# Performance work log

Hardware: AMD Instinct MI355X
Metric: run time of the kernel (lower is better)

The kernel has to match this reference:

```python
import jax, jax.numpy as jnp
import numpy as np


def _discretize(A, B, C, step):
    # Bilinear (Tustin) discretization, as in the source module.
    N = A.shape[0]
    I = jnp.eye(N, dtype=A.dtype)
    BL = jnp.linalg.inv(I - (step / 2.0) * A)
    Ab = BL @ (I + (step / 2.0) * A)
    Bb = (BL * step) @ B  # (N, 1)
    return Ab, Bb, C


def _k_conv(Ab, Bb, Cb, L):
    # K[l] = Cb @ Ab^l @ Bb, computed by a linear recurrence instead of
    # L explicit matrix powers (same math as the source's K_conv).
    def step(v, _):
        k = (Cb @ v)[0, 0]
        return Ab @ v, k

    _, K = jax.lax.scan(step, Bb, None, length=L)
    return K  # (L,)


def setup_inputs() -> dict:
    key = jax.random.key(0)
    k_u, k_a, k_b, k_c, k_s = jax.random.split(key, 5)
    N, L, BATCH = 64, 16384, 512
    u = jax.random.normal(k_u, (BATCH, L), dtype=jnp.float32)
    # lecun_normal inits: std = 1/sqrt(fan_in)
    A = jax.random.normal(k_a, (N, N), dtype=jnp.float32) / np.sqrt(N)
    B = jax.random.normal(k_b, (N, 1), dtype=jnp.float32)  # fan_in = 1
    C = jax.random.normal(k_c, (1, N), dtype=jnp.float32) / np.sqrt(N)
    D = jnp.ones((1,), dtype=jnp.float32)
    # log_step_initializer(dt_min=1e-3, dt_max=0.1)
    lo, hi = np.log(1e-3), np.log(0.1)
    log_step = (jax.random.uniform(k_s, (1,)) * (hi - lo) + lo).astype(jnp.float32)
    return {"u": u, "A": A, "B": B, "C": C, "D": D, "log_step": log_step}


def reference(u, A, B, C, D, log_step) -> jnp.ndarray:
    L = u.shape[-1]
    step = jnp.exp(log_step)  # (1,)
    Ab, Bb, Cb = _discretize(A, B, C, step)
    K = _k_conv(Ab, Bb, Cb, L)  # (L,)
    # FFT causal convolution: pad both signals to length 2L (as in source),
    # multiply in frequency domain, take first L samples.
    n = 2 * L
    ud = jnp.fft.rfft(u, n=n, axis=-1)          # (BATCH, L+1) complex
    Kd = jnp.fft.rfft(K, n=n)                   # (L+1,) complex, broadcast
    y = jnp.fft.irfft(ud * Kd, n=n, axis=-1)[..., :L]
    return y + D * u
```

## Files before the change

### kernel.cpp

```cpp
#include <hip/hip_runtime.h>
#include <cstddef>

typedef double f64x4 __attribute__((ext_vector_type(4)));
typedef float  f32x4 __attribute__((ext_vector_type(4)));
typedef short  bf16x8 __attribute__((ext_vector_type(8)));

static constexpr int RCN = 512 * 128;

static constexpr size_t WS_W  = 0;
static constexpr size_t WS_G  = 8192;
static constexpr size_t WS_MD = 32768;
static constexpr size_t WS_BV = 40960;
static constexpr size_t WS_X  = WS_BV + (size_t)RCN * 64;

__device__ __forceinline__ unsigned short f2bf(float f) {
  union { float f; unsigned u; } v; v.f = f;
  unsigned u = v.u + 0x7FFFu + ((v.u >> 16) & 1u);
  return (unsigned short)(u >> 16);
}

__device__ __forceinline__ double probeE(int i, int k) {
  return (double)(((i * 3 + k * 5) & 7) - 3);
}
__device__ __forceinline__ double probeF(int k, int j) {
  return (double)(((k * 7 + j * 2) & 7) - 4);
}

__device__ __forceinline__ bool probe_mfma_layout(int lr, int lq, int rowm[4], int* colm_out)
{
  f64x4 z; z[0] = 0.0; z[1] = 0.0; z[2] = 0.0; z[3] = 0.0;
  f64x4 p1 = __builtin_amdgcn_mfma_f64_16x16x4f64((double)lr, 1.0, z, 0, 0, 0);
  f64x4 p2 = __builtin_amdgcn_mfma_f64_16x16x4f64(1.0, (double)lr, z, 0, 0, 0);
  bool okl = true;
#pragma unroll
  for (int r = 0; r < 4; ++r) {
    int rr = (int)(p1[r] * 0.25 + 0.5);
    okl = okl && (p1[r] == 4.0 * (double)rr) && rr >= 0 && rr < 16;
    rowm[r] = rr & 15;
    okl = okl && (p2[r] == p2[0]);
  }
  int cc = (int)(p2[0] * 0.25 + 0.5);
  okl = okl && (p2[0] == 4.0 * (double)cc) && cc >= 0 && cc < 16;
  *colm_out = cc & 15;
  f64x4 d = __builtin_amdgcn_mfma_f64_16x16x4f64(probeE(lr, lq), probeF(lq, lr), z, 0, 0, 0);
#pragma unroll
  for (int r = 0; r < 4; ++r) {
    double ref = 0.0;
#pragma unroll
    for (int k = 0; k < 4; ++k) ref += probeE(rowm[r], k) * probeF(k, cc & 15);
    okl = okl && (d[r] == ref);
  }
  return __all(okl) != 0;
}

template<bool ADD>
__device__ __forceinline__ void mm64_mfma(const double* A, const double* B, double* D,
                                          int wi, int wj, int lr, int lq,
                                          const int rowm[4], int colm)
{
  f64x4 acc;
  if (ADD) {
#pragma unroll
    for (int r = 0; r < 4; ++r)
      acc[r] = D[(wi * 16 + rowm[r]) * 65 + wj * 16 + colm];
  } else {
    acc[0] = 0.0; acc[1] = 0.0; acc[2] = 0.0; acc[3] = 0.0;
  }
#pragma unroll
  for (int kb = 0; kb < 16; ++kb) {
    double a = A[(wi * 16 + lr) * 65 + kb * 4 + lq];
    double b = B[(kb * 4 + lq) * 65 + wj * 16 + lr];
    acc = __builtin_amdgcn_mfma_f64_16x16x4f64(a, b, acc, 0, 0, 0);
  }
  __syncthreads();
#pragma unroll
  for (int r = 0; r < 4; ++r)
    D[(wi * 16 + rowm[r]) * 65 + wj * 16 + colm] = acc[r];
  __syncthreads();
}

__device__ __forceinline__ void wh_tile(const float* Wf, const float* Hf,
                                        const double* Pd, float* Wo, float* Ho,
                                        int n, bool isW, int wi, int wj,
                                        int lr, int lq, const int rowm[4], int colm)
{
  f64x4 acc;
  acc[0] = 0.0; acc[1] = 0.0; acc[2] = 0.0; acc[3] = 0.0;
#pragma unroll
  for (int kb = 0; kb < 16; ++kb) {
    double a, b;
    if (isW) {
      a = (double)Wf[(wi * 16 + lr) * 65 + kb * 4 + lq];
      b = Pd[(wj * 16 + lr) * 65 + kb * 4 + lq];
    } else {
      a = (double)Hf[(wi * 16 + lr) * 65 + kb * 4 + lq];
      b = Pd[(kb * 4 + lq) * 65 + wj * 16 + lr];
    }
    acc = __builtin_amdgcn_mfma_f64_16x16x4f64(a, b, acc, 0, 0, 0);
  }
#pragma unroll
  for (int r = 0; r < 4; ++r) {
    int drow = wi * 16 + rowm[r];
    if (drow < n) {
      if (isW) Wo[(n + drow) * 65 + wj * 16 + colm] = (float)acc[r];
      else     Ho[(n + drow) * 65 + wj * 16 + colm] = (float)acc[r];
    }
  }
}

template<bool ADD>
__device__ __forceinline__ void mm64x2(const double* A, const double* B, double* D,
                                       int tr2, int tc2)
{
  double a00 = 0, a01 = 0, a10 = 0, a11 = 0;
#pragma unroll 8
  for (int c = 0; c < 64; ++c) {
    double av0 = A[(tr2 + 0) * 65 + c];
    double av1 = A[(tr2 + 1) * 65 + c];
    double bv0 = B[c * 65 + tc2 + 0];
    double bv1 = B[c * 65 + tc2 + 1];
    a00 = fma(av0, bv0, a00); a01 = fma(av0, bv1, a01);
    a10 = fma(av1, bv0, a10); a11 = fma(av1, bv1, a11);
  }
  double o00, o01, o10, o11;
  if (ADD) {
    o00 = D[(tr2 + 0) * 65 + tc2 + 0]; o01 = D[(tr2 + 0) * 65 + tc2 + 1];
    o10 = D[(tr2 + 1) * 65 + tc2 + 0]; o11 = D[(tr2 + 1) * 65 + tc2 + 1];
  }
  __syncthreads();
  D[(tr2 + 0) * 65 + tc2 + 0] = ADD ? (o00 + a00) : a00;
  D[(tr2 + 0) * 65 + tc2 + 1] = ADD ? (o01 + a01) : a01;
  D[(tr2 + 1) * 65 + tc2 + 0] = ADD ? (o10 + a10) : a10;
  D[(tr2 + 1) * 65 + tc2 + 1] = ADD ? (o11 + a11) : a11;
  __syncthreads();
}

__global__ __launch_bounds__(1024) void k_precomp(
    const float* __restrict__ Ain, const float* __restrict__ Bin,
    const float* __restrict__ Cin, const float* __restrict__ Din,
    const float* __restrict__ LS, float* ws)
{
  __shared__ double Xd[64 * 65];
  __shared__ double Pd[64 * 65];
  __shared__ float  Wf[128 * 65];
  __shared__ float  Hf[128 * 65];
  __shared__ float  Kf[128];

  const int t    = threadIdx.x;
  const int wave = t >> 6;
  const int lane = t & 63;
  const int lr   = lane & 15;
  const int lq   = lane >> 4;
  const int wv_i = wave >> 2;
  const int wv_j = wave & 3;
  const int tr2  = (t >> 5) << 1;
  const int tc2  = (t & 31) << 1;

  int rowm[4]; int colm;
  const bool use_mfma = probe_mfma_layout(lr, lq, rowm, &colm);

  unsigned short* Wtg = (unsigned short*)(ws + WS_W);
  unsigned short* Gtg = (unsigned short*)(ws + WS_G);
  double* Mgd = (double*)(ws + WS_MD);

  const double step = exp((double)LS[0]);
  const double h = 0.5 * step;

  for (int idx = t; idx < 4096; idx += 1024) {
    int i = idx >> 6, j = idx & 63;
    double a = h * (double)Ain[idx];
    Xd[i * 65 + j] = a;
    Pd[i * 65 + j] = a + ((i == j) ? 1.0 : 0.0);
  }
  __syncthreads();

  if (use_mfma) {
    for (int k = 0; k < 3; ++k) {
      mm64_mfma<false>(Xd, Xd, Xd, wv_i, wv_j, lr, lq, rowm, colm);
      mm64_mfma<true >(Pd, Xd, Pd, wv_i, wv_j, lr, lq, rowm, colm);
    }
  } else {
    for (int k = 0; k < 3; ++k) {
      mm64x2<false>(Xd, Xd, Xd, tr2, tc2);
      mm64x2<true >(Pd, Xd, Pd, tr2, tc2);
    }
  }

  if (t < 64) {
    double bb = 0.0;
    for (int c = 0; c < 64; ++c) bb = fma(Pd[t * 65 + c], (double)Bin[c], bb);
    Wf[t] = (float)(bb * step);
  }
  __syncthreads();

  for (int idx = t; idx < 4096; idx += 1024) {
    int i = idx >> 6, j = idx & 63;
    Pd[i * 65 + j] = 2.0 * Pd[i * 65 + j] - ((i == j) ? 1.0 : 0.0);
  }
  __syncthreads();

  if (t < 64) {
    double hh = 0.0;
    for (int c = 0; c < 64; ++c) hh = fma((double)Cin[c], Pd[c * 65 + t], hh);
    Hf[t] = (float)hh;
  }
  __syncthreads();

  if (use_mfma) {
    for (int k = 0; k < 7; ++k) {
      const int n     = 1 << k;
      const int tpm   = (n + 15) >> 4;
      const int tiles = tpm << 2;
      if (tiles <= 8) {
        if (wave < 2 * tiles) {
          const bool isW = wave < tiles;
          const int  w   = isW ? wave : wave - tiles;
          wh_tile(Wf, Hf, Pd, Wf, Hf, n, isW, w >> 2, w & 3, lr, lq, rowm, colm);
        }
      } else {
        wh_tile(Wf, Hf, Pd, Wf, Hf, n, true,  wv_i, wv_j, lr, lq, rowm, colm);
        wh_tile(Wf, Hf, Pd, Wf, Hf, n, false, wv_i, wv_j, lr, lq, rowm, colm);
      }
      mm64_mfma<false>(Pd, Pd, Pd, wv_i, wv_j, lr, lq, rowm, colm);
    }
  } else {
    for (int k = 0; k < 7; ++k) {
      const int n = 1 << k;
      if (n <= 16) {
        if (t < (n << 6)) {
          int r = t >> 6, ii = t & 63;
          double aw = 0.0, ah = 0.0;
#pragma unroll 4
          for (int c = 0; c < 64; ++c) {
            aw = fma(Pd[ii * 65 + c], (double)Wf[r * 65 + c], aw);
            ah = fma((double)Hf[r * 65 + c], Pd[c * 65 + ii], ah);
          }
          Wf[(n + r) * 65 + ii] = (float)aw;
          Hf[(n + r) * 65 + ii] = (float)ah;
        }
      } else if (n == 32) {
        const int r  = t >> 5;
        const int i2 = (t & 31) << 1;
        double w0 = 0, w1 = 0, h0 = 0, h1 = 0;
#pragma unroll 4
        for (int c = 0; c < 64; ++c) {
          double wr = (double)Wf[r * 65 + c];
          w0 = fma(wr, Pd[(i2 + 0) * 65 + c], w0);
          w1 = fma(wr, Pd[(i2 + 1) * 65 + c], w1);
          double hr = (double)Hf[r * 65 + c];
          h0 = fma(hr, Pd[c * 65 + i2 + 0], h0);
          h1 = fma(hr, Pd[c * 65 + i2 + 1], h1);
        }
        Wf[(32 + r) * 65 + i2 + 0] = (float)w0;
        Wf[(32 + r) * 65 + i2 + 1] = (float)w1;
        Hf[(32 + r) * 65 + i2 + 0] = (float)h0;
        Hf[(32 + r) * 65 + i2 + 1] = (float)h1;
      } else {
        const int r2 = tr2, i2 = tc2;
        double w00 = 0, w01 = 0, w10 = 0, w11 = 0;
        double h00 = 0, h01 = 0, h10 = 0, h11 = 0;
#pragma unroll 4
        for (int c = 0; c < 64; ++c) {
          double wa = (double)Wf[(r2 + 0) * 65 + c];
          double wb = (double)Wf[(r2 + 1) * 65 + c];
          double p0 = Pd[(i2 + 0) * 65 + c];
          double p1 = Pd[(i2 + 1) * 65 + c];
          w00 = fma(wa, p0, w00); w01 = fma(wa, p1, w01);
          w10 = fma(wb, p0, w10); w11 = fma(wb, p1, w11);
          double ha = (double)Hf[(r2 + 0) * 65 + c];
          double hb = (double)Hf[(r2 + 1) * 65 + c];
          double q0 = Pd[c * 65 + i2 + 0];
          double q1 = Pd[c * 65 + i2 + 1];
          h00 = fma(ha, q0, h00); h01 = fma(ha, q1, h01);
          h10 = fma(hb, q0, h10); h11 = fma(hb, q1, h11);
        }
        Wf[(64 + r2 + 0) * 65 + i2 + 0] = (float)w00;
        Wf[(64 + r2 + 0) * 65 + i2 + 1] = (float)w01;
        Wf[(64 + r2 + 1) * 65 + i2 + 0] = (float)w10;
        Wf[(64 + r2 + 1) * 65 + i2 + 1] = (float)w11;
        Hf[(64 + r2 + 0) * 65 + i2 + 0] = (float)h00;
        Hf[(64 + r2 + 0) * 65 + i2 + 1] = (float)h01;
        Hf[(64 + r2 + 1) * 65 + i2 + 0] = (float)h10;
        Hf[(64 + r2 + 1) * 65 + i2 + 1] = (float)h11;
      }
      mm64x2<false>(Pd, Pd, Pd, tr2, tc2);
    }
  }

  for (int idx = t; idx < 4096; idx += 1024)
    Mgd[idx] = Pd[(idx >> 6) * 65 + (idx & 63)];

  if (t < 128) {
    double s = 0.0;
    for (int c = 0; c < 64; ++c) s = fma((double)Cin[c], (double)Wf[t * 65 + c], s);
    Kf[t] = (float)s;
  }
  __syncthreads();

  for (int idx = t; idx < 8192; idx += 1024) {
    int i = idx >> 7, kk = idx & 127;
    Wtg[idx] = f2bf(Wf[(127 - kk) * 65 + i]);
  }

  const float Dval = Din[0];
  for (int idx = t; idx < 16384; idx += 1024) {
    int r = idx >> 7, kg = idx & 127;
    float v = (r >= kg) ? Kf[r - kg] : 0.f;
    if (kg == r) v += Dval;
    Gtg[r * 192 + kg] = f2bf(v);
  }
  for (int idx = t; idx < 8192; idx += 1024) {
    int r = idx >> 6, i = idx & 63;
    Gtg[r * 192 + 128 + i] = f2bf(Hf[r * 65 + i]);
  }
}

__global__ __launch_bounds__(256) void k_chunkvec(
    const float* __restrict__ u, const unsigned short* __restrict__ Wt,
    float* __restrict__ bout)
{
  __shared__ unsigned short Bs[64 * 136];
  __shared__ unsigned short As[128 * 40];
  const int t = threadIdx.x;
  const int rc0 = blockIdx.x << 7;
  const int w  = t >> 6;
  const int lane = t & 63;
  const int lr = lane & 15, lq = lane >> 4;

  {
    const unsigned* src = (const unsigned*)Wt;
    unsigned* dst = (unsigned*)Bs;
    for (int idx = t; idx < 4096; idx += 256) {
      int r = idx >> 6, c = idx & 63;
      dst[r * 68 + c] = src[idx];
    }
  }
  for (int it = t; it < 1024; it += 256) {
    int rcl = it >> 3, k4 = (it & 7) << 2;
    float4 v = *(const float4*)&u[((size_t)(rc0 + rcl) << 7) + k4];
    ushort4 s;
    s.x = f2bf(v.x); s.y = f2bf(v.y); s.z = f2bf(v.z); s.w = f2bf(v.w);
    *(ushort4*)&As[rcl * 40 + k4] = s;
  }
  __syncthreads();

  f32x4 acc[2][4];
#pragma unroll
  for (int i = 0; i < 2; ++i)
#pragma unroll
    for (int j = 0; j < 4; ++j) { acc[i][j][0] = 0.f; acc[i][j][1] = 0.f; acc[i][j][2] = 0.f; acc[i][j][3] = 0.f; }

  for (int sl = 0; sl < 4; ++sl) {
    bf16x8 av[2], bv[4];
#pragma unroll
    for (int ti = 0; ti < 2; ++ti)
      av[ti] = *(const bf16x8*)&As[(w * 32 + ti * 16 + lr) * 40 + lq * 8];
#pragma unroll
    for (int tj = 0; tj < 4; ++tj)
      bv[tj] = *(const bf16x8*)&Bs[(tj * 16 + lr) * 136 + sl * 32 + lq * 8];
#pragma unroll
    for (int ti = 0; ti < 2; ++ti)
#pragma unroll
      for (int tj = 0; tj < 4; ++tj)
        acc[ti][tj] = __builtin_amdgcn_mfma_f32_16x16x32_bf16(av[ti], bv[tj], acc[ti][tj], 0, 0, 0);
    if (sl < 3) {
      __syncthreads();
      for (int it = t; it < 1024; it += 256) {
        int rcl = it >> 3, k4 = (it & 7) << 2;
        float4 v = *(const float4*)&u[((size_t)(rc0 + rcl) << 7) + ((sl + 1) << 5) + k4];
        ushort4 s;
        s.x = f2bf(v.x); s.y = f2bf(v.y); s.z = f2bf(v.z); s.w = f2bf(v.w);
        *(ushort4*)&As[rcl * 40 + k4] = s;
      }
      __syncthreads();
    }
  }

#pragma unroll
  for (int ti = 0; ti < 2; ++ti)
#pragma unroll
    for (int tj = 0; tj < 4; ++tj)
#pragma unroll
      for (int r = 0; r < 4; ++r) {
        int row = rc0 + w * 32 + ti * 16 + lq * 4 + r;
        bout[((size_t)row << 6) + tj * 16 + lr] = acc[ti][tj][r];
      }
}

__global__ __launch_bounds__(64) void k_scan(
    const double* __restrict__ Mg, const float* __restrict__ bv,
    float* __restrict__ Xg)
{
  __shared__ float xs[64];
  const int lane = threadIdx.x;
  float Mr[64];
#pragma unroll
  for (int c = 0; c < 64; ++c)
    Mr[c] = (float)Mg[((size_t)lane << 6) + c];
  const float* br = bv + ((size_t)blockIdx.x << 13);
  float* Xr = Xg + ((size_t)blockIdx.x << 13);
  xs[lane] = 0.f;
  float bcur = br[lane];
  __syncthreads();
  for (int j = 0; j < 128; ++j) {
    float bnext = (j < 127) ? br[((j + 1) << 6) + lane] : 0.f;
    float y0 = 0.f, y1 = 0.f, y2 = 0.f, y3 = 0.f;
#pragma unroll
    for (int c4 = 0; c4 < 16; ++c4) {
      float4 xv = *(const float4*)&xs[c4 << 2];
      y0 = fmaf(Mr[c4 * 4 + 0], xv.x, y0);
      y1 = fmaf(Mr[c4 * 4 + 1], xv.y, y1);
      y2 = fmaf(Mr[c4 * 4 + 2], xv.z, y2);
      y3 = fmaf(Mr[c4 * 4 + 3], xv.w, y3);
    }
    float xold = xs[lane];
    Xr[(j << 6) + lane] = xold;
    float xnew = bcur + ((y0 + y1) + (y2 + y3));
    __syncthreads();
    xs[lane] = xnew;
    __syncthreads();
    bcur = bnext;
  }
}

__global__ __launch_bounds__(256) void k_main(
    const float* __restrict__ u, const float* __restrict__ Xg,
    const unsigned short* __restrict__ Gt, float* __restrict__ out)
{
  __shared__ unsigned short Gs[128 * 200];
  __shared__ unsigned short As[128 * 40];
  const int t = threadIdx.x;
  const int rc0 = blockIdx.x << 7;
  const int w  = t >> 6;
  const int lane = t & 63;
  const int lr = lane & 15, lq = lane >> 4;

  {
    const unsigned* src = (const unsigned*)Gt;
    unsigned* dst = (unsigned*)Gs;
    for (int idx = t; idx < 12288; idx += 256) {
      int r = idx / 96, c = idx - r * 96;
      dst[r * 100 + c] = src[idx];
    }
  }
  for (int it = t; it < 1024; it += 256) {
    int rcl = it >> 3, k4 = (it & 7) << 2;
    float4 v = *(const float4*)&u[((size_t)(rc0 + rcl) << 7) + k4];
    ushort4 s;
    s.x = f2bf(v.x); s.y = f2bf(v.y); s.z = f2bf(v.z); s.w = f2bf(v.w);
    *(ushort4*)&As[rcl * 40 + k4] = s;
  }
  __syncthreads();

  f32x4 acc[2][8];
#pragma unroll
  for (int i = 0; i < 2; ++i)
#pragma unroll
    for (int j = 0; j < 8; ++j) { acc[i][j][0] = 0.f; acc[i][j][1] = 0.f; acc[i][j][2] = 0.f; acc[i][j][3] = 0.f; }

  for (int sl = 0; sl < 6; ++sl) {
    bf16x8 av[2], bv[8];
#pragma unroll
    for (int ti = 0; ti < 2; ++ti)
      av[ti] = *(const bf16x8*)&As[(w * 32 + ti * 16 + lr) * 40 + lq * 8];
#pragma unroll
    for (int tj = 0; tj < 8; ++tj)
      bv[tj] = *(const bf16x8*)&Gs[(tj * 16 + lr) * 200 + sl * 32 + lq * 8];
#pragma unroll
    for (int ti = 0; ti < 2; ++ti)
#pragma unroll
      for (int tj = 0; tj < 8; ++tj)
        acc[ti][tj] = __builtin_amdgcn_mfma_f32_16x16x32_bf16(av[ti], bv[tj], acc[ti][tj], 0, 0, 0);
    if (sl < 5) {
      __syncthreads();
      for (int it = t; it < 1024; it += 256) {
        int rcl = it >> 3, k4 = (it & 7) << 2;
        int kg = ((sl + 1) << 5) + k4;
        float4 v;
        if (kg < 128)
          v = *(const float4*)&u[((size_t)(rc0 + rcl) << 7) + kg];
        else
          v = *(const float4*)&Xg[((size_t)(rc0 + rcl) << 6) + (kg - 128)];
        ushort4 s;
        s.x = f2bf(v.x); s.y = f2bf(v.y); s.z = f2bf(v.z); s.w = f2bf(v.w);
        *(ushort4*)&As[rcl * 40 + k4] = s;
      }
      __syncthreads();
    }
  }

#pragma unroll
  for (int ti = 0; ti < 2; ++ti)
#pragma unroll
    for (int tj = 0; tj < 8; ++tj)
#pragma unroll
      for (int r = 0; r < 4; ++r) {
        int row = rc0 + w * 32 + ti * 16 + lq * 4 + r;
        out[((size_t)row << 7) + tj * 16 + lr] = acc[ti][tj][r];
      }
}

extern "C" void kernel_launch(void* const* d_in, const int* in_sizes, int n_in,
                              void* d_out, int out_size, void* d_ws, size_t ws_size,
                              hipStream_t stream) {
  (void)in_sizes; (void)n_in; (void)out_size; (void)ws_size;
  const float* u  = (const float*)d_in[0];
  const float* A  = (const float*)d_in[1];
  const float* Bv = (const float*)d_in[2];
  const float* Cv = (const float*)d_in[3];
  const float* Dv = (const float*)d_in[4];
  const float* ls = (const float*)d_in[5];
  float* out = (float*)d_out;
  float* ws  = (float*)d_ws;

  k_precomp<<<1, 1024, 0, stream>>>(A, Bv, Cv, Dv, ls, ws);
  k_chunkvec<<<512, 256, 0, stream>>>(u, (const unsigned short*)(ws + WS_W), ws + WS_BV);
  k_scan<<<512, 64, 0, stream>>>((const double*)(ws + WS_MD), ws + WS_BV, ws + WS_X);
  k_main<<<512, 256, 0, stream>>>(u, ws + WS_X, (const unsigned short*)(ws + WS_G), out);
}
```

Baseline: 220.5 us.

## Halve serial chunk scan depth via squared transition matrix and pairwise combining

The chunk-state scan now pairs adjacent chunks. Each pair is combined in parallel with M, then a single wave runs a 64-step serial recurrence using M^2, which is precomputed in k_precomp. Odd states are reconstructed in parallel afterwards. Cross-lane access uses readlane instead of shared-memory syncs, and the block uses 256 threads with chunk inputs staged in LDS. M is now stored as float rather than double, which lowers precision slightly, and the squared matrix adds some rounding error.

```diff
diff --git a/kernel.cpp b/kernel.cpp
--- a/kernel.cpp
+++ b/kernel.cpp
@@ -161,7 +161,7 @@
 
   unsigned short* Wtg = (unsigned short*)(ws + WS_W);
   unsigned short* Gtg = (unsigned short*)(ws + WS_G);
-  double* Mgd = (double*)(ws + WS_MD);
+  float* Mf = ws + WS_MD;
 
   const double step = exp((double)LS[0]);
   const double h = 0.5 * step;
@@ -288,7 +288,12 @@
   }
 
   for (int idx = t; idx < 4096; idx += 1024)
-    Mgd[idx] = Pd[(idx >> 6) * 65 + (idx & 63)];
+    Mf[idx] = (float)Pd[(idx >> 6) * 65 + (idx & 63)];
+
+  if (use_mfma) mm64_mfma<false>(Pd, Pd, Pd, wv_i, wv_j, lr, lq, rowm, colm);
+  else          mm64x2<false>(Pd, Pd, Pd, tr2, tc2);
+  for (int idx = t; idx < 4096; idx += 1024)
+    Mf[4096 + idx] = (float)Pd[(idx >> 6) * 65 + (idx & 63)];
 
   if (t < 128) {
     double s = 0.0;
@@ -387,39 +392,78 @@
       }
 }
 
-__global__ __launch_bounds__(64) void k_scan(
-    const double* __restrict__ Mg, const float* __restrict__ bv,
-    float* __restrict__ Xg)
-{
-  __shared__ float xs[64];
-  const int lane = threadIdx.x;
-  float Mr[64];
-#pragma unroll
-  for (int c = 0; c < 64; ++c)
-    Mr[c] = (float)Mg[((size_t)lane << 6) + c];
+__global__ __launch_bounds__(256) void k_scan(
+    const float* __restrict__ Mf,
+    const float* __restrict__ bv, float* __restrict__ Xg)
+{
+  __shared__ float bs[128 * 64];
+  __shared__ float ds[64 * 64];
+  __shared__ float xs[64 * 64];
+  const int t = threadIdx.x, w = t >> 6, lane = t & 63;
   const float* br = bv + ((size_t)blockIdx.x << 13);
   float* Xr = Xg + ((size_t)blockIdx.x << 13);
-  xs[lane] = 0.f;
-  float bcur = br[lane];
-  __syncthreads();
-  for (int j = 0; j < 128; ++j) {
-    float bnext = (j < 127) ? br[((j + 1) << 6) + lane] : 0.f;
+
+  for (int it = t; it < 2048; it += 256)
+    ((float4*)bs)[it] = ((const float4*)br)[it];
+
+  float Mr[64], M2r[64];
+#pragma unroll
+  for (int c4 = 0; c4 < 16; ++c4) {
+    *(float4*)&Mr[c4 * 4]  = *(const float4*)&Mf[(lane << 6) + c4 * 4];
+    *(float4*)&M2r[c4 * 4] = *(const float4*)&Mf[4096 + (lane << 6) + c4 * 4];
+  }
+  __syncthreads();
+
+  for (int k = 0; k < 16; ++k) {
+    const int tp = (w << 4) + k;
     float y0 = 0.f, y1 = 0.f, y2 = 0.f, y3 = 0.f;
 #pragma unroll
     for (int c4 = 0; c4 < 16; ++c4) {
-      float4 xv = *(const float4*)&xs[c4 << 2];
-      y0 = fmaf(Mr[c4 * 4 + 0], xv.x, y0);
-      y1 = fmaf(Mr[c4 * 4 + 1], xv.y, y1);
-      y2 = fmaf(Mr[c4 * 4 + 2], xv.z, y2);
-      y3 = fmaf(Mr[c4 * 4 + 3], xv.w, y3);
-    }
-    float xold = xs[lane];
-    Xr[(j << 6) + lane] = xold;
-    float xnew = bcur + ((y0 + y1) + (y2 + y3));
-    __syncthreads();
-    xs[lane] = xnew;
-    __syncthreads();
-    bcur = bnext;
+      float4 bb = *(const float4*)&bs[((tp << 1) << 6) + (c4 << 2)];
+      y0 = fmaf(Mr[c4 * 4 + 0], bb.x, y0);
+      y1 = fmaf(Mr[c4 * 4 + 1], bb.y, y1);
+      y2 = fmaf(Mr[c4 * 4 + 2], bb.z, y2);
+      y3 = fmaf(Mr[c4 * 4 + 3], bb.w, y3);
+    }
+    ds[(tp << 6) + lane] = ((y0 + y1) + (y2 + y3)) + bs[(((tp << 1) + 1) << 6) + lane];
+  }
+  __syncthreads();
+
+  if (w == 0) {
+    float x = 0.f;
+    float ecur = ds[lane];
+    for (int u = 0; u < 64; ++u) {
+      xs[(u << 6) + lane] = x;
+      float en = (u < 63) ? ds[((u + 1) << 6) + lane] : 0.f;
+      const unsigned xb = __float_as_uint(x);
+      float y0 = 0.f, y1 = 0.f, y2 = 0.f, y3 = 0.f;
+#pragma unroll
+      for (int c = 0; c < 64; c += 4) {
+        y0 = fmaf(M2r[c + 0], __uint_as_float(__builtin_amdgcn_readlane(xb, c + 0)), y0);
+        y1 = fmaf(M2r[c + 1], __uint_as_float(__builtin_amdgcn_readlane(xb, c + 1)), y1);
+        y2 = fmaf(M2r[c + 2], __uint_as_float(__builtin_amdgcn_readlane(xb, c + 2)), y2);
+        y3 = fmaf(M2r[c + 3], __uint_as_float(__builtin_amdgcn_readlane(xb, c + 3)), y3);
+      }
+      x = ((y0 + y1) + (y2 + y3)) + ecur;
+      ecur = en;
+    }
+  }
+  __syncthreads();
+
+  for (int k = 0; k < 16; ++k) {
+    const int tp = (w << 4) + k;
+    Xr[((tp << 1) << 6) + lane] = xs[(tp << 6) + lane];
+    float y0 = 0.f, y1 = 0.f, y2 = 0.f, y3 = 0.f;
+#pragma unroll
+    for (int c4 = 0; c4 < 16; ++c4) {
+      float4 xx = *(const float4*)&xs[(tp << 6) + (c4 << 2)];
+      y0 = fmaf(Mr[c4 * 4 + 0], xx.x, y0);
+      y1 = fmaf(Mr[c4 * 4 + 1], xx.y, y1);
+      y2 = fmaf(Mr[c4 * 4 + 2], xx.z, y2);
+      y3 = fmaf(Mr[c4 * 4 + 3], xx.w, y3);
+    }
+    Xr[(((tp << 1) + 1) << 6) + lane] =
+        ((y0 + y1) + (y2 + y3)) + bs[((tp << 1) << 6) + lane];
   }
 }
 
@@ -515,6 +559,6 @@
 
   k_precomp<<<1, 1024, 0, stream>>>(A, Bv, Cv, Dv, ls, ws);
   k_chunkvec<<<512, 256, 0, stream>>>(u, (const unsigned short*)(ws + WS_W), ws + WS_BV);
-  k_scan<<<512, 64, 0, stream>>>((const double*)(ws + WS_MD), ws + WS_BV, ws + WS_X);
+  k_scan<<<512, 256, 0, stream>>>(ws + WS_MD, ws + WS_BV, ws + WS_X);
   k_main<<<512, 256, 0, stream>>>(u, ws + WS_X, (const unsigned short*)(ws + WS_G), out);
 }
```

New measurement: 211.1 us. 1.04x faster.
